# Kernel optimization log

Measured on AMD Instinct MI355X. Metric: run time of the kernel, lower is better.

Reference implementation:

```python
import jax, jax.numpy as jnp
from jax import lax
import numpy as np

B, C_IN, C_OUT, H, W = 4, 256, 256, 4, 8192
HD = C_OUT // H          # head_dim = 64
K_ATT = 7
PAD = (1 * (K_ATT - 1) + 1) // 2  # = 3 (dilation=1)
CK = 1                   # conv_kernel_size (must be 1 for the module's shapes to be consistent)


def setup_inputs() -> dict:
    key = jax.random.key(0)
    ks = jax.random.split(key, 14)
    s = 0.05
    inp = {
        "x": jax.random.normal(ks[0], (B, C_IN, W), dtype=jnp.float32),
        # 1x1 convs q/k/v: weight [C_out, C_in], bias [C_out]
        "w1": jax.random.normal(ks[1], (C_OUT, C_IN), dtype=jnp.float32) * (C_IN ** -0.5),
        "b1": jax.random.normal(ks[2], (C_OUT,), dtype=jnp.float32) * s,
        "w2": jax.random.normal(ks[3], (C_OUT, C_IN), dtype=jnp.float32) * (C_IN ** -0.5),
        "b2": jax.random.normal(ks[4], (C_OUT,), dtype=jnp.float32) * s,
        "w3": jax.random.normal(ks[5], (C_OUT, C_IN), dtype=jnp.float32) * (C_IN ** -0.5),
        "b3": jax.random.normal(ks[6], (C_OUT,), dtype=jnp.float32) * s,
        # conv_p: Conv1d(1, head_dim, 1): weight [HD], bias [HD]
        "wp": jax.random.normal(ks[7], (HD,), dtype=jnp.float32) * s,
        "bp": jax.random.normal(ks[8], (HD,), dtype=jnp.float32) * s,
        # fc: Conv2d(3*H, CK, 1, bias=False): weight [CK, 3H]
        "fc_w": jax.random.normal(ks[9], (CK, 3 * H), dtype=jnp.float32) * ((3 * H) ** -0.5),
        # dep_conv: Conv1d(CK*HD -> C_OUT, kernel=CK, groups=HD): weight [C_OUT, CK, CK], bias [C_OUT]
        "dep_w": jax.random.normal(ks[10], (C_OUT, CK, CK), dtype=jnp.float32) * s,
        "dep_b": jax.random.normal(ks[11], (C_OUT,), dtype=jnp.float32) * s,
        "rate1": jnp.float32(0.5),
        "rate2": jnp.float32(0.5),
    }
    return inp


def _conv1x1(x, w, b):  # x: [B, Cin, W] -> [B, Cout, W]
    return jnp.einsum('oc,bcw->bow', w, x) + b[None, :, None]


def _unfold(p):  # p: [..., Wp] -> windows [..., W, K_ATT]
    idx = jnp.arange(W)[:, None] + jnp.arange(K_ATT)[None, :]
    return p[..., idx]


def _forward(x, w1, b1, w2, b2, w3, b3, wp, bp, fc_w, dep_w, dep_b, rate1, rate2):
    q = _conv1x1(x, w1, b1)   # [B, C, W]
    k = _conv1x1(x, w2, b2)
    v = _conv1x1(x, w3, b3)
    scaling = HD ** -0.5

    # positional encoding: conv_p(linspace(-1,1,W)) -> [HD, W]
    loc = jnp.linspace(-1.0, 1.0, W, dtype=jnp.float32)
    pe = wp[:, None] * loc[None, :] + bp[:, None]

    q_att = q.reshape(B * H, HD, W) * scaling
    k_att = k.reshape(B * H, HD, W)
    v_att = v.reshape(B * H, HD, W)

    # reflection pad last axis by PAD, then unfold to [.., HD, W, K]
    pad3 = lambda t: jnp.pad(t, ((0, 0), (0, 0), (PAD, PAD)), mode='reflect')
    uk = _unfold(pad3(k_att))                                   # [BH, HD, W, K]
    uv = _unfold(pad3(v_att))                                   # [BH, HD, W, K]
    upe = _unfold(jnp.pad(pe, ((0, 0), (PAD, PAD)), mode='reflect'))  # [HD, W, K]

    # att = sum_d q * (unfold_k + q_pe - unfold_rpe); softmax over window K
    D = pe[:, :, None] - upe                                     # [HD, W, K]
    att = jnp.einsum('bdw,bdwk->bwk', q_att, uk + D[None])       # [BH, W, K]
    att = jax.nn.softmax(att, axis=-1)
    out_att = jnp.einsum('bwk,bdwk->bdw', att, uv).reshape(B, C_OUT, W)

    # conv branch: fc over concatenated heads, then grouped dep_conv
    qkv = jnp.concatenate([q.reshape(B, H, HD, W),
                           k.reshape(B, H, HD, W),
                           v.reshape(B, H, HD, W)], axis=1)      # [B, 3H, HD, W]
    f_all = jnp.einsum('oc,bcdw->bodw', fc_w, qkv)               # [B, CK, HD, W]
    f_conv = jnp.transpose(f_all, (0, 2, 1, 3)).reshape(B, HD * CK, W)
    out_conv = lax.conv_general_dilated(
        f_conv, dep_w, window_strides=(1,), padding='VALID',
        dimension_numbers=('NCH', 'OIH', 'NCH'), feature_group_count=HD)
    out_conv = out_conv + dep_b[None, :, None]

    return rate1 * out_att + rate2 * out_conv


def reference(x, w1, b1, w2, b2, w3, b3, wp, bp, fc_w, dep_w, dep_b, rate1, rate2):
    return _forward(x, w1, b1, w2, b2, w3, b3, wp, bp, fc_w, dep_w, dep_b, rate1, rate2)
```

## Files before the change

kernel.cpp:

```cpp
#include <hip/hip_runtime.h>
#include <stdint.h>
#include <stddef.h>

typedef unsigned short u16;
typedef unsigned int   u32;

typedef __attribute__((ext_vector_type(8))) short bf16x8;
typedef __attribute__((ext_vector_type(4))) float f32x4;

__device__ __forceinline__ float b2f(u16 u)    { return __uint_as_float(((u32)u) << 16); }
__device__ __forceinline__ float b2f_lo(u32 v) { return __uint_as_float(v << 16); }
__device__ __forceinline__ float b2f_hi(u32 v) { return __uint_as_float(v & 0xFFFF0000u); }
__device__ __forceinline__ u16 f2b(float f){
  u32 x = __float_as_uint(f);
  return (u16)((x + 0x7FFFu + ((x >> 16) & 1u)) >> 16);
}

__global__ __launch_bounds__(256) void k_transpose(const float* __restrict__ x, u16* __restrict__ xt){
  __shared__ u16 tile[64 * 65];
  const int wt = blockIdx.x, ct = blockIdx.y, b = blockIdx.z;
  const int W0 = wt << 6, C0 = ct << 6;
  const int t = threadIdx.x;
#pragma unroll
  for (int it = 0; it < 4; ++it){
    const int task = t + (it << 8);
    const int c = task >> 4, u = task & 15;
    const float4 d = *(const float4*)(x + ((size_t)((b << 8) + C0 + c) << 13) + W0 + (u << 2));
    const int base = c * 65 + (u << 2);
    tile[base + 0] = f2b(d.x); tile[base + 1] = f2b(d.y);
    tile[base + 2] = f2b(d.z); tile[base + 3] = f2b(d.w);
  }
  __syncthreads();
#pragma unroll
  for (int it = 0; it < 2; ++it){
    const int task = t + (it << 8);
    const int wr = task >> 3, cu = task & 7;
    const int cb = cu << 3;
    u32 a0 = (u32)tile[(cb + 0) * 65 + wr] | ((u32)tile[(cb + 1) * 65 + wr] << 16);
    u32 a1 = (u32)tile[(cb + 2) * 65 + wr] | ((u32)tile[(cb + 3) * 65 + wr] << 16);
    u32 a2 = (u32)tile[(cb + 4) * 65 + wr] | ((u32)tile[(cb + 5) * 65 + wr] << 16);
    u32 a3 = (u32)tile[(cb + 6) * 65 + wr] | ((u32)tile[(cb + 7) * 65 + wr] << 16);
    uint4 val = make_uint4(a0, a1, a2, a3);
    *(uint4*)(xt + ((size_t)((b << 13) + W0 + wr) << 8) + C0 + cb) = val;
  }
}

__global__ __launch_bounds__(256) void k_build(const float* __restrict__ w1, const float* __restrict__ b1,
                                               const float* __restrict__ w2, const float* __restrict__ b2,
                                               const float* __restrict__ w3, const float* __restrict__ b3,
                                               const float* __restrict__ fcw,
                                               u16* __restrict__ Wall, float* __restrict__ ball){
  const int r = blockIdx.x, c = threadIdx.x;
  float v = 0.f, bv = 0.f;
  if (r < 256){      v = w1[(r << 8) + c];          bv = b1[r]; }
  else if (r < 512){ v = w2[((r - 256) << 8) + c];  bv = b2[r - 256]; }
  else if (r < 768){ v = w3[((r - 512) << 8) + c];  bv = b3[r - 512]; }
  else if (r < 832){
    const int d = r - 768;
    float s = 0.f, sbias = 0.f;
#pragma unroll
    for (int h = 0; h < 4; ++h){
      const int ch = (h << 6) + d;
      const float f1 = fcw[h], f2 = fcw[4 + h], f3 = fcw[8 + h];
      s     += f1 * w1[(ch << 8) + c] + f2 * w2[(ch << 8) + c] + f3 * w3[(ch << 8) + c];
      sbias += f1 * b1[ch] + f2 * b2[ch] + f3 * b3[ch];
    }
    v = s; bv = sbias;
  }
  Wall[(r << 8) + c] = f2b(v);
  if (c == 0) ball[r] = bv;
}

__global__ __launch_bounds__(256) void gemm_qkv(const u16* __restrict__ Wall, const float* __restrict__ ball,
                                                const u16* __restrict__ xt, u16* __restrict__ qkvt){
  __shared__ __align__(16) u16 As[128 * 64];
  __shared__ __align__(16) u16 Bs[128 * 64];
  const int mt = blockIdx.x, nt = blockIdx.y;
  const int b = nt >> 6;
  const int w0 = (nt & 63) << 7;
  const int tid = threadIdx.x;
  const int wave = tid >> 6, lane = tid & 63;
  const int wy = wave >> 1, wx = wave & 1;
  const int m0 = mt << 7;
  const int quad = lane >> 4, l15 = lane & 15;
  f32x4 acc[4][4] = {};

  for (int kc = 0; kc < 256; kc += 64){
    uint4 ra[4], rb[4];
#pragma unroll
    for (int k = 0; k < 4; ++k){
      const int cid = tid + (k << 8);
      const int row = cid >> 3, u = cid & 7;
      ra[k] = *(const uint4*)(Wall + ((m0 + row) << 8) + kc + (u << 3));
      rb[k] = *(const uint4*)(xt + (((size_t)((b << 13) + w0 + row)) << 8) + kc + (u << 3));
    }
    __syncthreads();
#pragma unroll
    for (int k = 0; k < 4; ++k){
      const int cid = tid + (k << 8);
      const int row = cid >> 3, u = cid & 7;
      *(uint4*)(As + (row << 6) + (u << 3)) = ra[k];
      *(uint4*)(Bs + (row << 6) + (u << 3)) = rb[k];
    }
    __syncthreads();
#pragma unroll
    for (int ks = 0; ks < 2; ++ks){
      bf16x8 av[4], bvv[4];
#pragma unroll
      for (int i = 0; i < 4; ++i){
        const int rowA = (wy << 6) + (i << 4) + l15;
        av[i] = *(const bf16x8*)(As + (rowA << 6) + (((ks << 2) + quad) << 3));
        const int rowB = (wx << 6) + (i << 4) + l15;
        bvv[i] = *(const bf16x8*)(Bs + (rowB << 6) + (((ks << 2) + quad) << 3));
      }
#pragma unroll
      for (int i = 0; i < 4; ++i)
#pragma unroll
        for (int j = 0; j < 4; ++j)
          acc[i][j] = __builtin_amdgcn_mfma_f32_16x16x32_bf16(av[i], bvv[j], acc[i][j], 0, 0, 0);
    }
  }

#pragma unroll
  for (int i = 0; i < 4; ++i){
    const int m = m0 + (wy << 6) + (i << 4) + (quad << 2);
    if (m < 832){
      const float4 bias = *(const float4*)(ball + m);
#pragma unroll
      for (int j = 0; j < 4; ++j){
        const int w = w0 + (wx << 6) + (j << 4) + l15;
        f32x4 r = acc[i][j];
        u32 lo = (u32)f2b(r.x + bias.x) | ((u32)f2b(r.y + bias.y) << 16);
        u32 hi = (u32)f2b(r.z + bias.z) | ((u32)f2b(r.w + bias.w) << 16);
        uint2 val; val.x = lo; val.y = hi;
        *(uint2*)(qkvt + ((size_t)((b << 13) + w)) * 832 + m) = val;
      }
    }
  }
}

__global__ __launch_bounds__(256) void attn_out(const u16* __restrict__ qkvt, const float* __restrict__ wp,
                                                const float* __restrict__ depw, const float* __restrict__ depb,
                                                const float* __restrict__ r1p, const float* __restrict__ r2p,
                                                float* __restrict__ out){
  __shared__ __align__(16) u16 sb[262 * 32];
  __shared__ float wpL[64];
  const int wt = blockIdx.x, h = blockIdx.y, b = blockIdx.z;
  const int w0 = wt << 8;
  const int t = threadIdx.x;
  const int w = w0 + t;
  if (t < 64) wpL[t] = wp[t];

  const u16* rowp = qkvt + ((size_t)((b << 13) + w)) * 832;
  uint4 qreg[8];
#pragma unroll
  for (int j = 0; j < 8; ++j) qreg[j] = *(const uint4*)(rowp + (h << 6) + (j << 3));
  float fv[16];
  {
    uint4 f0 = *(const uint4*)(rowp + 768 + (h << 4));
    uint4 f1 = *(const uint4*)(rowp + 768 + (h << 4) + 8);
    fv[0] = b2f_lo(f0.x); fv[1] = b2f_hi(f0.x); fv[2]  = b2f_lo(f0.y); fv[3]  = b2f_hi(f0.y);
    fv[4] = b2f_lo(f0.z); fv[5] = b2f_hi(f0.z); fv[6]  = b2f_lo(f0.w); fv[7]  = b2f_hi(f0.w);
    fv[8] = b2f_lo(f1.x); fv[9] = b2f_hi(f1.x); fv[10] = b2f_lo(f1.y); fv[11] = b2f_hi(f1.y);
    fv[12]= b2f_lo(f1.z); fv[13]= b2f_hi(f1.z); fv[14] = b2f_lo(f1.w); fv[15] = b2f_hi(f1.w);
  }

  float att[7] = {0.f,0.f,0.f,0.f,0.f,0.f,0.f};
  float qd = 0.f;

#pragma unroll
  for (int half = 0; half < 2; ++half){
    __syncthreads();
    for (int idx = t; idx < 262 * 4; idx += 256){
      const int row = idx >> 2, u = idx & 3;
      int wsrc = w0 - 3 + row;
      wsrc = wsrc < 0 ? -wsrc : (wsrc > 8191 ? 16382 - wsrc : wsrc);
      const uint4 d = *(const uint4*)(qkvt + ((size_t)((b << 13) + wsrc)) * 832 + 256 + (h << 6) + (half << 5) + (u << 3));
      *(uint4*)(sb + (row << 5) + (((u + (row >> 1)) & 3) << 3)) = d;
    }
    __syncthreads();
#pragma unroll
    for (int jj = 0; jj < 4; ++jj){
      const int j = (half << 2) + jj;
      float qf[8];
      {
        const uint4 q4 = qreg[j];
        qf[0] = b2f_lo(q4.x); qf[1] = b2f_hi(q4.x); qf[2] = b2f_lo(q4.y); qf[3] = b2f_hi(q4.y);
        qf[4] = b2f_lo(q4.z); qf[5] = b2f_hi(q4.z); qf[6] = b2f_lo(q4.w); qf[7] = b2f_hi(q4.w);
      }
#pragma unroll
      for (int e = 0; e < 8; ++e) qd += qf[e] * wpL[(j << 3) + e];
#pragma unroll
      for (int kk = 0; kk < 7; ++kk){
        const int r = t + kk;
        const uint4 kv = *(const uint4*)(sb + (r << 5) + (((jj + (r >> 1)) & 3) << 3));
        float a = att[kk];
        a += qf[0] * b2f_lo(kv.x) + qf[1] * b2f_hi(kv.x) + qf[2] * b2f_lo(kv.y) + qf[3] * b2f_hi(kv.y)
           + qf[4] * b2f_lo(kv.z) + qf[5] * b2f_hi(kv.z) + qf[6] * b2f_lo(kv.w) + qf[7] * b2f_hi(kv.w);
        att[kk] = a;
      }
    }
  }

  const float locw = -1.f + (2.f / 8191.f) * (float)w;
  float mx = -1e30f;
#pragma unroll
  for (int kk = 0; kk < 7; ++kk){
    int wr = w + kk - 3;
    wr = wr < 0 ? -wr : (wr > 8191 ? 16382 - wr : wr);
    const float lr = -1.f + (2.f / 8191.f) * (float)wr;
    att[kk] = 0.125f * (att[kk] + (locw - lr) * qd);
    mx = fmaxf(mx, att[kk]);
  }
  float p[7]; float ssum = 0.f;
#pragma unroll
  for (int kk = 0; kk < 7; ++kk){ p[kk] = __expf(att[kk] - mx); ssum += p[kk]; }
  const float inv = 1.f / ssum;
#pragma unroll
  for (int kk = 0; kk < 7; ++kk) p[kk] *= inv;

  const float r1 = r1p[0];
  const float r2 = r2p[0];

#pragma unroll
  for (int half = 0; half < 2; ++half){
    __syncthreads();
    for (int idx = t; idx < 262 * 4; idx += 256){
      const int row = idx >> 2, u = idx & 3;
      int wsrc = w0 - 3 + row;
      wsrc = wsrc < 0 ? -wsrc : (wsrc > 8191 ? 16382 - wsrc : wsrc);
      const uint4 d = *(const uint4*)(qkvt + ((size_t)((b << 13) + wsrc)) * 832 + 512 + (h << 6) + (half << 5) + (u << 3));
      *(uint4*)(sb + (row << 5) + (((u + (row >> 1)) & 3) << 3)) = d;
    }
    __syncthreads();
#pragma unroll
    for (int jj = 0; jj < 4; ++jj){
      float o[8] = {0.f,0.f,0.f,0.f,0.f,0.f,0.f,0.f};
#pragma unroll
      for (int kk = 0; kk < 7; ++kk){
        const int r = t + kk;
        const uint4 vv = *(const uint4*)(sb + (r << 5) + (((jj + (r >> 1)) & 3) << 3));
        const float pk = p[kk];
        o[0] += pk * b2f_lo(vv.x); o[1] += pk * b2f_hi(vv.x);
        o[2] += pk * b2f_lo(vv.y); o[3] += pk * b2f_hi(vv.y);
        o[4] += pk * b2f_lo(vv.z); o[5] += pk * b2f_hi(vv.z);
        o[6] += pk * b2f_lo(vv.w); o[7] += pk * b2f_hi(vv.w);
      }
      const int dl0 = (half << 5) + (jj << 3);
#pragma unroll
      for (int e = 0; e < 8; ++e){
        const int dl = dl0 + e;
        const float oc = depw[(h << 6) + dl] * fv[dl >> 2] + depb[(h << 6) + dl];
        out[(((size_t)((b << 8) + (h << 6) + dl)) << 13) + w] = r1 * o[e] + r2 * oc;
      }
    }
  }
}

extern "C" void kernel_launch(void* const* d_in, const int* in_sizes, int n_in,
                              void* d_out, int out_size, void* d_ws, size_t ws_size,
                              hipStream_t stream){
  (void)in_sizes; (void)n_in; (void)out_size; (void)ws_size;
  const float* x    = (const float*)d_in[0];
  const float* w1   = (const float*)d_in[1];
  const float* b1   = (const float*)d_in[2];
  const float* w2   = (const float*)d_in[3];
  const float* b2   = (const float*)d_in[4];
  const float* w3   = (const float*)d_in[5];
  const float* b3   = (const float*)d_in[6];
  const float* wp   = (const float*)d_in[7];
  const float* fcw  = (const float*)d_in[9];
  const float* depw = (const float*)d_in[10];
  const float* depb = (const float*)d_in[11];
  const float* r1p  = (const float*)d_in[12];
  const float* r2p  = (const float*)d_in[13];
  float* out = (float*)d_out;

  char* ws = (char*)d_ws;
  u16*   xt   = (u16*)(ws);
  u16*   Wall = (u16*)(ws + 16777216);
  float* ball = (float*)(ws + 17235968);
  u16*   qkvt = (u16*)(ws + 17239552);

  k_transpose<<<dim3(128, 4, 4), 256, 0, stream>>>(x, xt);
  k_build<<<dim3(896, 1, 1), 256, 0, stream>>>(w1, b1, w2, b2, w3, b3, fcw, Wall, ball);
  gemm_qkv<<<dim3(7, 256, 1), 256, 0, stream>>>(Wall, ball, xt, qkvt);
  attn_out<<<dim3(32, 4, 4), 256, 0, stream>>>(qkvt, wp, depw, depb, r1p, r2p, out);
}
```

Measured before the change: 230.1 us.

## Prefetch, swizzle LDS, coalesce stores, and remap blocks in QKV GEMM

The QKV GEMM now prefetches the next K-chunk of global data into registers while MFMAs run on the current chunk. It XOR-swizzles the LDS layout to avoid bank conflicts on the bf16x8 fragment reads. The epilogue stages the output tile through LDS so each thread writes a 16-byte row segment instead of a scattered 8-byte store. A 1D grid with a remapped block order is meant to improve L2 locality across XCDs. These changes add register pressure and extra LDS traffic in the epilogue. The bias read for padded rows beyond 832 now happens unguarded, though it appears to stay within the allocated region.

```diff
diff --git a/kernel.cpp b/kernel.cpp
--- a/kernel.cpp
+++ b/kernel.cpp
@@ -73,9 +73,14 @@
 
 __global__ __launch_bounds__(256) void gemm_qkv(const u16* __restrict__ Wall, const float* __restrict__ ball,
                                                 const u16* __restrict__ xt, u16* __restrict__ qkvt){
-  __shared__ __align__(16) u16 As[128 * 64];
-  __shared__ __align__(16) u16 Bs[128 * 64];
-  const int mt = blockIdx.x, nt = blockIdx.y;
+  __shared__ __align__(16) u16 sm[2 * 128 * 64];
+  u16* As = sm;
+  u16* Bs = sm + 128 * 64;
+
+  const int bid = blockIdx.x;
+  const int w_id = ((bid & 7) * 224) + (bid >> 3);
+  const int mt = w_id % 7;
+  const int nt = w_id / 7;
   const int b = nt >> 6;
   const int w0 = (nt & 63) << 7;
   const int tid = threadIdx.x;
@@ -85,8 +90,8 @@
   const int quad = lane >> 4, l15 = lane & 15;
   f32x4 acc[4][4] = {};
 
-  for (int kc = 0; kc < 256; kc += 64){
-    uint4 ra[4], rb[4];
+  uint4 ra[4], rb[4];
+  auto stage_load = [&](int kc){
 #pragma unroll
     for (int k = 0; k < 4; ++k){
       const int cid = tid + (k << 8);
@@ -94,24 +99,32 @@
       ra[k] = *(const uint4*)(Wall + ((m0 + row) << 8) + kc + (u << 3));
       rb[k] = *(const uint4*)(xt + (((size_t)((b << 13) + w0 + row)) << 8) + kc + (u << 3));
     }
+  };
+
+  stage_load(0);
+#pragma unroll
+  for (int kt = 0; kt < 4; ++kt){
     __syncthreads();
 #pragma unroll
     for (int k = 0; k < 4; ++k){
       const int cid = tid + (k << 8);
-      const int row = cid >> 3, u = cid & 7;
+      const int row = cid >> 3, u = (cid & 7) ^ (row & 7);
       *(uint4*)(As + (row << 6) + (u << 3)) = ra[k];
       *(uint4*)(Bs + (row << 6) + (u << 3)) = rb[k];
     }
     __syncthreads();
+    if (kt < 3) stage_load((kt + 1) << 6);
 #pragma unroll
     for (int ks = 0; ks < 2; ++ks){
       bf16x8 av[4], bvv[4];
 #pragma unroll
       for (int i = 0; i < 4; ++i){
         const int rowA = (wy << 6) + (i << 4) + l15;
-        av[i] = *(const bf16x8*)(As + (rowA << 6) + (((ks << 2) + quad) << 3));
+        const int ca = ((ks << 2) + quad) ^ (rowA & 7);
+        av[i] = *(const bf16x8*)(As + (rowA << 6) + (ca << 3));
         const int rowB = (wx << 6) + (i << 4) + l15;
-        bvv[i] = *(const bf16x8*)(Bs + (rowB << 6) + (((ks << 2) + quad) << 3));
+        const int cb2 = ((ks << 2) + quad) ^ (rowB & 7);
+        bvv[i] = *(const bf16x8*)(Bs + (rowB << 6) + (cb2 << 3));
       }
 #pragma unroll
       for (int i = 0; i < 4; ++i)
@@ -121,20 +134,32 @@
     }
   }
 
+  __syncthreads();
 #pragma unroll
   for (int i = 0; i < 4; ++i){
-    const int m = m0 + (wy << 6) + (i << 4) + (quad << 2);
-    if (m < 832){
-      const float4 bias = *(const float4*)(ball + m);
-#pragma unroll
-      for (int j = 0; j < 4; ++j){
-        const int w = w0 + (wx << 6) + (j << 4) + l15;
-        f32x4 r = acc[i][j];
-        u32 lo = (u32)f2b(r.x + bias.x) | ((u32)f2b(r.y + bias.y) << 16);
-        u32 hi = (u32)f2b(r.z + bias.z) | ((u32)f2b(r.w + bias.w) << 16);
-        uint2 val; val.x = lo; val.y = hi;
-        *(uint2*)(qkvt + ((size_t)((b << 13) + w)) * 832 + m) = val;
-      }
+    const int ml = (wy << 6) + (i << 4) + (quad << 2);
+    const float4 bias = *(const float4*)(ball + m0 + ml);
+#pragma unroll
+    for (int j = 0; j < 4; ++j){
+      const int wl = (wx << 6) + (j << 4) + l15;
+      f32x4 r = acc[i][j];
+      uint2 val;
+      val.x = (u32)f2b(r.x + bias.x) | ((u32)f2b(r.y + bias.y) << 16);
+      val.y = (u32)f2b(r.z + bias.z) | ((u32)f2b(r.w + bias.w) << 16);
+      const int byte = ((wl << 8) + (ml << 1)) ^ ((wl & 7) << 4);
+      *(uint2*)((char*)sm + byte) = val;
+    }
+  }
+  __syncthreads();
+#pragma unroll
+  for (int it = 0; it < 8; ++it){
+    const int task = tid + (it << 8);
+    const int wl = task >> 4, c = task & 15;
+    const int mcol = m0 + (c << 3);
+    if (mcol < 832){
+      const int byte = ((wl << 8) + (c << 4)) ^ ((wl & 7) << 4);
+      const uint4 val = *(const uint4*)((const char*)sm + byte);
+      *(uint4*)(qkvt + ((size_t)((b << 13) + w0 + wl)) * 832 + mcol) = val;
     }
   }
 }
@@ -284,6 +309,6 @@
 
   k_transpose<<<dim3(128, 4, 4), 256, 0, stream>>>(x, xt);
   k_build<<<dim3(896, 1, 1), 256, 0, stream>>>(w1, b1, w2, b2, w3, b3, fcw, Wall, ball);
-  gemm_qkv<<<dim3(7, 256, 1), 256, 0, stream>>>(Wall, ball, xt, qkvt);
+  gemm_qkv<<<dim3(1792, 1, 1), 256, 0, stream>>>(Wall, ball, xt, qkvt);
   attn_out<<<dim3(32, 4, 4), 256, 0, stream>>>(qkvt, wp, depw, depb, r1p, r2p, out);
 }
```

After: 219.0 us. 4.8% less time.

## Fuse transpose, QKV GEMM and windowed attention into one stripe kernel

Applied to the files above, without the earlier changes.

Replaces the transpose, GEMM and attention kernels with a single kernel per 64-column stripe. The kernel loads x with a halo directly into LDS as bf16, runs all seven M-tiles of the projection GEMM against it, and writes Q, K/V and the fc projection into swizzled LDS buffers before computing the 7-tap attention and the conv branch. This removes the global round trip of the transposed x and the 832-wide qkv intermediate. In exchange it recomputes the halo rows, uses heavy LDS (one block per CU), and processes heads per thread-group instead of per block.

```diff
diff --git a/kernel.cpp b/kernel.cpp
--- a/kernel.cpp
+++ b/kernel.cpp
@@ -8,41 +8,16 @@
 typedef __attribute__((ext_vector_type(8))) short bf16x8;
 typedef __attribute__((ext_vector_type(4))) float f32x4;
 
-__device__ __forceinline__ float b2f(u16 u)    { return __uint_as_float(((u32)u) << 16); }
 __device__ __forceinline__ float b2f_lo(u32 v) { return __uint_as_float(v << 16); }
 __device__ __forceinline__ float b2f_hi(u32 v) { return __uint_as_float(v & 0xFFFF0000u); }
 __device__ __forceinline__ u16 f2b(float f){
   u32 x = __float_as_uint(f);
   return (u16)((x + 0x7FFFu + ((x >> 16) & 1u)) >> 16);
 }
-
-__global__ __launch_bounds__(256) void k_transpose(const float* __restrict__ x, u16* __restrict__ xt){
-  __shared__ u16 tile[64 * 65];
-  const int wt = blockIdx.x, ct = blockIdx.y, b = blockIdx.z;
-  const int W0 = wt << 6, C0 = ct << 6;
-  const int t = threadIdx.x;
-#pragma unroll
-  for (int it = 0; it < 4; ++it){
-    const int task = t + (it << 8);
-    const int c = task >> 4, u = task & 15;
-    const float4 d = *(const float4*)(x + ((size_t)((b << 8) + C0 + c) << 13) + W0 + (u << 2));
-    const int base = c * 65 + (u << 2);
-    tile[base + 0] = f2b(d.x); tile[base + 1] = f2b(d.y);
-    tile[base + 2] = f2b(d.z); tile[base + 3] = f2b(d.w);
-  }
-  __syncthreads();
-#pragma unroll
-  for (int it = 0; it < 2; ++it){
-    const int task = t + (it << 8);
-    const int wr = task >> 3, cu = task & 7;
-    const int cb = cu << 3;
-    u32 a0 = (u32)tile[(cb + 0) * 65 + wr] | ((u32)tile[(cb + 1) * 65 + wr] << 16);
-    u32 a1 = (u32)tile[(cb + 2) * 65 + wr] | ((u32)tile[(cb + 3) * 65 + wr] << 16);
-    u32 a2 = (u32)tile[(cb + 4) * 65 + wr] | ((u32)tile[(cb + 5) * 65 + wr] << 16);
-    u32 a3 = (u32)tile[(cb + 6) * 65 + wr] | ((u32)tile[(cb + 7) * 65 + wr] << 16);
-    uint4 val = make_uint4(a0, a1, a2, a3);
-    *(uint4*)(xt + ((size_t)((b << 13) + W0 + wr) << 8) + C0 + cb) = val;
-  }
+__device__ __forceinline__ int refl(int w){ return w < 0 ? -w : (w > 8191 ? 16382 - w : w); }
+__device__ __forceinline__ void up8(const uint4 v, float* f){
+  f[0] = b2f_lo(v.x); f[1] = b2f_hi(v.x); f[2] = b2f_lo(v.y); f[3] = b2f_hi(v.y);
+  f[4] = b2f_lo(v.z); f[5] = b2f_hi(v.z); f[6] = b2f_lo(v.w); f[7] = b2f_hi(v.w);
 }
 
 __global__ __launch_bounds__(256) void k_build(const float* __restrict__ w1, const float* __restrict__ b1,
@@ -71,134 +46,172 @@
   if (c == 0) ball[r] = bv;
 }
 
-__global__ __launch_bounds__(256) void gemm_qkv(const u16* __restrict__ Wall, const float* __restrict__ ball,
-                                                const u16* __restrict__ xt, u16* __restrict__ qkvt){
-  __shared__ __align__(16) u16 As[128 * 64];
-  __shared__ __align__(16) u16 Bs[128 * 64];
-  const int mt = blockIdx.x, nt = blockIdx.y;
-  const int b = nt >> 6;
-  const int w0 = (nt & 63) << 7;
-  const int tid = threadIdx.x;
-  const int wave = tid >> 6, lane = tid & 63;
-  const int wy = wave >> 1, wx = wave & 1;
-  const int m0 = mt << 7;
+__global__ __launch_bounds__(256, 1) void fused_acmix(
+    const u16* __restrict__ Wall, const float* __restrict__ ball,
+    const float* __restrict__ x, const float* __restrict__ wp,
+    const float* __restrict__ depw, const float* __restrict__ depb,
+    const float* __restrict__ r1p, const float* __restrict__ r2p,
+    float* __restrict__ out)
+{
+  __shared__ __align__(16) u16 Bl [80 * 256];
+  __shared__ __align__(16) u16 As [128 * 64];
+  __shared__ __align__(16) u16 Ql [64 * 256];
+  __shared__ __align__(16) u16 KVl[70 * 512];
+  __shared__ float wpL[64];
+  u16* Fl = As;
+
+  const int bid = blockIdx.x;
+  const int w_id = ((bid & 7) << 6) + (bid >> 3);
+  const int b = w_id >> 7;
+  const int stripe = w_id & 127;
+  const int w0 = stripe << 6;
+
+  const int t = threadIdx.x;
+  const int wv = t >> 6, lane = t & 63;
   const int quad = lane >> 4, l15 = lane & 15;
-  f32x4 acc[4][4] = {};
-
-  for (int kc = 0; kc < 256; kc += 64){
-    uint4 ra[4], rb[4];
-#pragma unroll
-    for (int k = 0; k < 4; ++k){
-      const int cid = tid + (k << 8);
-      const int row = cid >> 3, u = cid & 7;
-      ra[k] = *(const uint4*)(Wall + ((m0 + row) << 8) + kc + (u << 3));
-      rb[k] = *(const uint4*)(xt + (((size_t)((b << 13) + w0 + row)) << 8) + kc + (u << 3));
-    }
-    __syncthreads();
-#pragma unroll
-    for (int k = 0; k < 4; ++k){
-      const int cid = tid + (k << 8);
-      const int row = cid >> 3, u = cid & 7;
-      *(uint4*)(As + (row << 6) + (u << 3)) = ra[k];
-      *(uint4*)(Bs + (row << 6) + (u << 3)) = rb[k];
-    }
-    __syncthreads();
-#pragma unroll
-    for (int ks = 0; ks < 2; ++ks){
-      bf16x8 av[4], bvv[4];
-#pragma unroll
-      for (int i = 0; i < 4; ++i){
-        const int rowA = (wy << 6) + (i << 4) + l15;
-        av[i] = *(const bf16x8*)(As + (rowA << 6) + (((ks << 2) + quad) << 3));
-        const int rowB = (wx << 6) + (i << 4) + l15;
-        bvv[i] = *(const bf16x8*)(Bs + (rowB << 6) + (((ks << 2) + quad) << 3));
-      }
-#pragma unroll
-      for (int i = 0; i < 4; ++i)
-#pragma unroll
-        for (int j = 0; j < 4; ++j)
-          acc[i][j] = __builtin_amdgcn_mfma_f32_16x16x32_bf16(av[i], bvv[j], acc[i][j], 0, 0, 0);
-    }
-  }
-
-#pragma unroll
-  for (int i = 0; i < 4; ++i){
-    const int m = m0 + (wy << 6) + (i << 4) + (quad << 2);
-    if (m < 832){
-      const float4 bias = *(const float4*)(ball + m);
-#pragma unroll
-      for (int j = 0; j < 4; ++j){
-        const int w = w0 + (wx << 6) + (j << 4) + l15;
-        f32x4 r = acc[i][j];
-        u32 lo = (u32)f2b(r.x + bias.x) | ((u32)f2b(r.y + bias.y) << 16);
-        u32 hi = (u32)f2b(r.z + bias.z) | ((u32)f2b(r.w + bias.w) << 16);
-        uint2 val; val.x = lo; val.y = hi;
-        *(uint2*)(qkvt + ((size_t)((b << 13) + w)) * 832 + m) = val;
-      }
-    }
-  }
-}
-
-__global__ __launch_bounds__(256) void attn_out(const u16* __restrict__ qkvt, const float* __restrict__ wp,
-                                                const float* __restrict__ depw, const float* __restrict__ depb,
-                                                const float* __restrict__ r1p, const float* __restrict__ r2p,
-                                                float* __restrict__ out){
-  __shared__ __align__(16) u16 sb[262 * 32];
-  __shared__ float wpL[64];
-  const int wt = blockIdx.x, h = blockIdx.y, b = blockIdx.z;
-  const int w0 = wt << 8;
-  const int t = threadIdx.x;
-  const int w = w0 + t;
+
   if (t < 64) wpL[t] = wp[t];
 
-  const u16* rowp = qkvt + ((size_t)((b << 13) + w)) * 832;
-  uint4 qreg[8];
-#pragma unroll
-  for (int j = 0; j < 8; ++j) qreg[j] = *(const uint4*)(rowp + (h << 6) + (j << 3));
-  float fv[16];
   {
-    uint4 f0 = *(const uint4*)(rowp + 768 + (h << 4));
-    uint4 f1 = *(const uint4*)(rowp + 768 + (h << 4) + 8);
-    fv[0] = b2f_lo(f0.x); fv[1] = b2f_hi(f0.x); fv[2]  = b2f_lo(f0.y); fv[3]  = b2f_hi(f0.y);
-    fv[4] = b2f_lo(f0.z); fv[5] = b2f_hi(f0.z); fv[6]  = b2f_lo(f0.w); fv[7]  = b2f_hi(f0.w);
-    fv[8] = b2f_lo(f1.x); fv[9] = b2f_hi(f1.x); fv[10] = b2f_lo(f1.y); fv[11] = b2f_hi(f1.y);
-    fv[12]= b2f_lo(f1.z); fv[13]= b2f_hi(f1.z); fv[14] = b2f_lo(f1.w); fv[15] = b2f_hi(f1.w);
-  }
+    const float* xb = x + ((size_t)b << 21);
+    const int cg = wv;
+    const int rl = lane;
+#pragma unroll
+    for (int ci = 0; ci < 8; ++ci){
+      const int cc = cg + (ci << 2);
+#pragma unroll
+      for (int rb = 0; rb < 2; ++rb){
+        const int r = rl + (rb << 6);
+        if (r < 80){
+          const int w = refl(w0 - 4 + r);
+          u32 pk0, pk1, pk2, pk3;
+          {
+            const size_t base = ((size_t)(cc << 3)) << 13;
+            const float f0 = xb[base + (0u << 13) + w];
+            const float f1 = xb[base + (1u << 13) + w];
+            const float f2 = xb[base + (2u << 13) + w];
+            const float f3 = xb[base + (3u << 13) + w];
+            const float f4 = xb[base + (4u << 13) + w];
+            const float f5 = xb[base + (5u << 13) + w];
+            const float f6 = xb[base + (6u << 13) + w];
+            const float f7 = xb[base + (7u << 13) + w];
+            pk0 = (u32)f2b(f0) | ((u32)f2b(f1) << 16);
+            pk1 = (u32)f2b(f2) | ((u32)f2b(f3) << 16);
+            pk2 = (u32)f2b(f4) | ((u32)f2b(f5) << 16);
+            pk3 = (u32)f2b(f6) | ((u32)f2b(f7) << 16);
+          }
+          *(uint4*)((char*)Bl + r * 512 + ((cc ^ (r & 31)) << 4)) = make_uint4(pk0, pk1, pk2, pk3);
+        }
+      }
+    }
+  }
+
+  uint4 ra[4];
+  auto loadA = [&](int mt_, int kc_){
+#pragma unroll
+    for (int k4 = 0; k4 < 4; ++k4){
+      const int task = t + (k4 << 8);
+      const int row = task >> 3, u = task & 7;
+      ra[k4] = *(const uint4*)(Wall + (((mt_ << 7) + row) << 8) + (kc_ << 6) + (u << 3));
+    }
+  };
+  loadA(0, 0);
+
+#pragma unroll
+  for (int mt = 0; mt < 7; ++mt){
+    f32x4 acc[2][5] = {};
+#pragma unroll
+    for (int kc = 0; kc < 4; ++kc){
+      __syncthreads();
+#pragma unroll
+      for (int k4 = 0; k4 < 4; ++k4){
+        const int task = t + (k4 << 8);
+        const int row = task >> 3, u = (task & 7) ^ (row & 7);
+        *(uint4*)((char*)As + row * 128 + (u << 4)) = ra[k4];
+      }
+      __syncthreads();
+      {
+        const int idx = (mt << 2) + kc;
+        if (idx < 27) loadA((idx + 1) >> 2, (idx + 1) & 3);
+      }
+#pragma unroll
+      for (int ks = 0; ks < 2; ++ks){
+        bf16x8 av[2], bv[5];
+#pragma unroll
+        for (int i = 0; i < 2; ++i){
+          const int rowA = (wv << 5) + (i << 4) + l15;
+          const int ca = ((ks << 2) + quad) ^ (rowA & 7);
+          av[i] = *(const bf16x8*)((const char*)As + rowA * 128 + (ca << 4));
+        }
+#pragma unroll
+        for (int j = 0; j < 5; ++j){
+          const int rowB = (j << 4) + l15;
+          const int cb = ((kc << 3) + (ks << 2) + quad) ^ (rowB & 31);
+          bv[j] = *(const bf16x8*)((const char*)Bl + rowB * 512 + (cb << 4));
+        }
+#pragma unroll
+        for (int i = 0; i < 2; ++i)
+#pragma unroll
+          for (int j = 0; j < 5; ++j)
+            acc[i][j] = __builtin_amdgcn_mfma_f32_16x16x32_bf16(av[i], bv[j], acc[i][j], 0, 0, 0);
+      }
+    }
+
+    if (mt == 6) __syncthreads();
+#pragma unroll
+    for (int i = 0; i < 2; ++i){
+      const int mloc = (wv << 5) + (i << 4) + (quad << 2);
+      const float4 bias = *(const float4*)(ball + (mt << 7) + mloc);
+#pragma unroll
+      for (int j = 0; j < 5; ++j){
+        const int r = (j << 4) + l15;
+        f32x4 c = acc[i][j];
+        uint2 val;
+        val.x = (u32)f2b(c.x + bias.x) | ((u32)f2b(c.y + bias.y) << 16);
+        val.y = (u32)f2b(c.z + bias.z) | ((u32)f2b(c.w + bias.w) << 16);
+        if (mt < 2){
+          const int wl = r - 4;
+          if ((unsigned)wl < 64u){
+            const int chunk = ((mt << 7) + mloc) >> 3;
+            *(uint2*)((char*)Ql + wl * 512 + ((chunk ^ (wl & 31)) << 4) + ((quad & 1) << 3)) = val;
+          }
+        } else if (mt < 6){
+          const int rr = r - 1;
+          if ((unsigned)rr < 70u){
+            const int chunk = (((mt - 2) << 7) + mloc) >> 3;
+            *(uint2*)((char*)KVl + rr * 1024 + ((chunk ^ (rr & 31)) << 4) + ((quad & 1) << 3)) = val;
+          }
+        } else {
+          const int wl = r - 4;
+          if ((unsigned)wl < 64u && mloc < 64){
+            const int chunk = mloc >> 3;
+            *(uint2*)((char*)Fl + wl * 128 + ((chunk ^ (wl & 7)) << 4) + ((quad & 1) << 3)) = val;
+          }
+        }
+      }
+    }
+  }
+  __syncthreads();
+
+  const int h = t >> 6, wl = t & 63;
+  const int w = w0 + wl;
 
   float att[7] = {0.f,0.f,0.f,0.f,0.f,0.f,0.f};
   float qd = 0.f;
-
-#pragma unroll
-  for (int half = 0; half < 2; ++half){
-    __syncthreads();
-    for (int idx = t; idx < 262 * 4; idx += 256){
-      const int row = idx >> 2, u = idx & 3;
-      int wsrc = w0 - 3 + row;
-      wsrc = wsrc < 0 ? -wsrc : (wsrc > 8191 ? 16382 - wsrc : wsrc);
-      const uint4 d = *(const uint4*)(qkvt + ((size_t)((b << 13) + wsrc)) * 832 + 256 + (h << 6) + (half << 5) + (u << 3));
-      *(uint4*)(sb + (row << 5) + (((u + (row >> 1)) & 3) << 3)) = d;
-    }
-    __syncthreads();
-#pragma unroll
-    for (int jj = 0; jj < 4; ++jj){
-      const int j = (half << 2) + jj;
-      float qf[8];
-      {
-        const uint4 q4 = qreg[j];
-        qf[0] = b2f_lo(q4.x); qf[1] = b2f_hi(q4.x); qf[2] = b2f_lo(q4.y); qf[3] = b2f_hi(q4.y);
-        qf[4] = b2f_lo(q4.z); qf[5] = b2f_hi(q4.z); qf[6] = b2f_lo(q4.w); qf[7] = b2f_hi(q4.w);
-      }
-#pragma unroll
-      for (int e = 0; e < 8; ++e) qd += qf[e] * wpL[(j << 3) + e];
-#pragma unroll
-      for (int kk = 0; kk < 7; ++kk){
-        const int r = t + kk;
-        const uint4 kv = *(const uint4*)(sb + (r << 5) + (((jj + (r >> 1)) & 3) << 3));
-        float a = att[kk];
-        a += qf[0] * b2f_lo(kv.x) + qf[1] * b2f_hi(kv.x) + qf[2] * b2f_lo(kv.y) + qf[3] * b2f_hi(kv.y)
-           + qf[4] * b2f_lo(kv.z) + qf[5] * b2f_hi(kv.z) + qf[6] * b2f_lo(kv.w) + qf[7] * b2f_hi(kv.w);
-        att[kk] = a;
-      }
+#pragma unroll
+  for (int e = 0; e < 8; ++e){
+    const int cq = (h << 3) + e;
+    const uint4 q4 = *(const uint4*)((const char*)Ql + wl * 512 + ((cq ^ (wl & 31)) << 4));
+    float qf[8]; up8(q4, qf);
+#pragma unroll
+    for (int d = 0; d < 8; ++d) qd += qf[d] * wpL[(e << 3) + d];
+#pragma unroll
+    for (int kk = 0; kk < 7; ++kk){
+      const int rr = wl + kk;
+      const uint4 k4 = *(const uint4*)((const char*)KVl + rr * 1024 + ((((h << 3) + e) ^ (rr & 31)) << 4));
+      float kf[8]; up8(k4, kf);
+      att[kk] += qf[0]*kf[0] + qf[1]*kf[1] + qf[2]*kf[2] + qf[3]*kf[3]
+               + qf[4]*kf[4] + qf[5]*kf[5] + qf[6]*kf[6] + qf[7]*kf[7];
     }
   }
 
@@ -206,8 +219,7 @@
   float mx = -1e30f;
 #pragma unroll
   for (int kk = 0; kk < 7; ++kk){
-    int wr = w + kk - 3;
-    wr = wr < 0 ? -wr : (wr > 8191 ? 16382 - wr : wr);
+    const int wr = refl(w + kk - 3);
     const float lr = -1.f + (2.f / 8191.f) * (float)wr;
     att[kk] = 0.125f * (att[kk] + (locw - lr) * qd);
     mx = fmaxf(mx, att[kk]);
@@ -219,40 +231,34 @@
 #pragma unroll
   for (int kk = 0; kk < 7; ++kk) p[kk] *= inv;
 
+  float fvv[16];
+  {
+    const int c0 = h << 1;
+    const uint4 f0 = *(const uint4*)((const char*)Fl + wl * 128 + ((c0 ^ (wl & 7)) << 4));
+    const uint4 f1 = *(const uint4*)((const char*)Fl + wl * 128 + (((c0 + 1) ^ (wl & 7)) << 4));
+    up8(f0, fvv); up8(f1, fvv + 8);
+  }
+
   const float r1 = r1p[0];
   const float r2 = r2p[0];
 
 #pragma unroll
-  for (int half = 0; half < 2; ++half){
-    __syncthreads();
-    for (int idx = t; idx < 262 * 4; idx += 256){
-      const int row = idx >> 2, u = idx & 3;
-      int wsrc = w0 - 3 + row;
-      wsrc = wsrc < 0 ? -wsrc : (wsrc > 8191 ? 16382 - wsrc : wsrc);
-      const uint4 d = *(const uint4*)(qkvt + ((size_t)((b << 13) + wsrc)) * 832 + 512 + (h << 6) + (half << 5) + (u << 3));
-      *(uint4*)(sb + (row << 5) + (((u + (row >> 1)) & 3) << 3)) = d;
-    }
-    __syncthreads();
-#pragma unroll
-    for (int jj = 0; jj < 4; ++jj){
-      float o[8] = {0.f,0.f,0.f,0.f,0.f,0.f,0.f,0.f};
-#pragma unroll
-      for (int kk = 0; kk < 7; ++kk){
-        const int r = t + kk;
-        const uint4 vv = *(const uint4*)(sb + (r << 5) + (((jj + (r >> 1)) & 3) << 3));
-        const float pk = p[kk];
-        o[0] += pk * b2f_lo(vv.x); o[1] += pk * b2f_hi(vv.x);
-        o[2] += pk * b2f_lo(vv.y); o[3] += pk * b2f_hi(vv.y);
-        o[4] += pk * b2f_lo(vv.z); o[5] += pk * b2f_hi(vv.z);
-        o[6] += pk * b2f_lo(vv.w); o[7] += pk * b2f_hi(vv.w);
-      }
-      const int dl0 = (half << 5) + (jj << 3);
-#pragma unroll
-      for (int e = 0; e < 8; ++e){
-        const int dl = dl0 + e;
-        const float oc = depw[(h << 6) + dl] * fv[dl >> 2] + depb[(h << 6) + dl];
-        out[(((size_t)((b << 8) + (h << 6) + dl)) << 13) + w] = r1 * o[e] + r2 * oc;
-      }
+  for (int e = 0; e < 8; ++e){
+    float o8[8] = {0.f,0.f,0.f,0.f,0.f,0.f,0.f,0.f};
+#pragma unroll
+    for (int kk = 0; kk < 7; ++kk){
+      const int rr = wl + kk;
+      const uint4 v4 = *(const uint4*)((const char*)KVl + rr * 1024 + (((32 + (h << 3) + e) ^ (rr & 31)) << 4));
+      float vf[8]; up8(v4, vf);
+      const float pk = p[kk];
+      o8[0] += pk * vf[0]; o8[1] += pk * vf[1]; o8[2] += pk * vf[2]; o8[3] += pk * vf[3];
+      o8[4] += pk * vf[4]; o8[5] += pk * vf[5]; o8[6] += pk * vf[6]; o8[7] += pk * vf[7];
+    }
+#pragma unroll
+    for (int s = 0; s < 8; ++s){
+      const int dl = (e << 3) + s;
+      const float oc = depw[(h << 6) + dl] * fvv[dl >> 2] + depb[(h << 6) + dl];
+      out[(((size_t)((b << 8) + (h << 6) + dl)) << 13) + w] = r1 * o8[s] + r2 * oc;
     }
   }
 }
@@ -277,13 +283,9 @@
   float* out = (float*)d_out;
 
   char* ws = (char*)d_ws;
-  u16*   xt   = (u16*)(ws);
-  u16*   Wall = (u16*)(ws + 16777216);
-  float* ball = (float*)(ws + 17235968);
-  u16*   qkvt = (u16*)(ws + 17239552);
-
-  k_transpose<<<dim3(128, 4, 4), 256, 0, stream>>>(x, xt);
+  u16*   Wall = (u16*)(ws);
+  float* ball = (float*)(ws + 458752);
+
   k_build<<<dim3(896, 1, 1), 256, 0, stream>>>(w1, b1, w2, b2, w3, b3, fcw, Wall, ball);
-  gemm_qkv<<<dim3(7, 256, 1), 256, 0, stream>>>(Wall, ball, xt, qkvt);
-  attn_out<<<dim3(32, 4, 4), 256, 0, stream>>>(qkvt, wp, depw, depb, r1p, r2p, out);
-}
+  fused_acmix<<<dim3(512, 1, 1), 256, 0, stream>>>(Wall, ball, x, wp, depw, depb, r1p, r2p, out);
+}
```

New measurement: 214.7 us. -6.7%, faster.
